# Optimization experiments

Measured on AMD Instinct MI355X. Metric: run time of the kernel, lower is better.

## Reference

```python
import jax, jax.numpy as jnp
import numpy as np

SIGMA = (2.0, 5.0, 10.0, 20.0, 40.0, 60.0)  # RBF bandwidths from __init__
MAX_SEG = 16  # static upper bound on number of class segments (== n classes in gt)


def setup_inputs() -> dict:
    key = jax.random.key(0)
    k1, k2, k3 = jax.random.split(key, 3)
    B, C, H, W = 1, 128, 64, 64
    predict = jax.random.normal(k1, (B, C, H, W), dtype=jnp.float32)
    target = jax.random.normal(k2, (B, C, H, W), dtype=jnp.float32)
    # sorted_randint -> contiguous variable-size class segments, as the torch loop assumes
    gt = jnp.sort(jax.random.randint(k3, (B * H * W,), 0, MAX_SEG)).reshape(B, H, W)
    ignore_mask = jnp.ones((B, H, W), dtype=bool)  # all pixels visible
    return {"predict": predict, "target": target, "gt": gt, "ignore_mask": ignore_mask}


def _sqdist(a, b):
    # ||a_i - b_j||^2 ; prob_mat in the original is -0.5 * this
    aa = jnp.sum(a * a, axis=1)
    bb = jnp.sum(b * b, axis=1)
    return aa[:, None] + bb[None, :] - 2.0 * (a @ b.T)


def reference(predict, target, gt, ignore_mask):
    d = predict.shape[1]
    # [B,C,H,W] -> [V,C]; ignore_mask is all True so visible set == all pixels
    pf = predict.transpose(0, 2, 3, 1).reshape(-1, d)
    tf = target.transpose(0, 2, 3, 1).reshape(-1, d)
    cls = gt.reshape(-1)

    # segment id = index of contiguous class run (what the Python boundary loop computes)
    boundary = (cls[1:] != cls[:-1]).astype(jnp.int32)
    seg = jnp.concatenate([jnp.zeros((1,), jnp.int32), jnp.cumsum(boundary)])
    counts = jax.ops.segment_sum(jnp.ones(seg.shape, predict.dtype), seg, num_segments=MAX_SEG)

    # pairwise squared distances within/between predict and target (shared across segments)
    Dpp = _sqdist(pf, pf)
    Dtt = _sqdist(tf, tf)
    Dpt = _sqdist(pf, tf)

    # Per segment with M=N=n: ww is +1/(2n^2) on pp/tt blocks, -1/(2n^2) on cross blocks,
    # and sum over the tp block equals sum over the pt block. So
    # loss_s = (1/(2 n^2)) * sum_bw sum_{i,j in s} (Kpp + Ktt - 2 Kpt)_{ij}
    C = jnp.zeros_like(Dpp)
    for bw in SIGMA:
        inv = -0.5 / bw  # K = exp(prob/bw) = exp(-||x_i-x_j||^2 / (2 bw))
        C = C + jnp.exp(inv * Dpp) + jnp.exp(inv * Dtt) - 2.0 * jnp.exp(inv * Dpt)

    same = seg[:, None] == seg[None, :]
    C = jnp.where(same, C, 0.0)
    seg_tot = jax.ops.segment_sum(jnp.sum(C, axis=1), seg, num_segments=MAX_SEG)

    denom = jnp.maximum(2.0 * counts * counts, 1.0)
    loss_s = jnp.where(counts > 0, seg_tot / denom, 0.0)
    pos = loss_s > 0
    loss_s = jnp.where(pos, jnp.sqrt(jnp.where(pos, loss_s, 1.0)), 0.0)  # sqrt(loss) if >0 else 0

    class_count = jnp.sum(counts > 0).astype(predict.dtype)
    return jnp.sum(loss_s) / class_count
```

## Files before the change

### kernel.cpp

```cpp
#include <hip/hip_runtime.h>
#include <math.h>

#define NCLS 16
#define TS   64
#define CH   32
#define PAD  36
#define NB   512
#define PIXB 16

typedef float vfloat4 __attribute__((ext_vector_type(4), aligned(4)));

struct Ctl {
    int   counts[NCLS];
    int   starts[NCLS + 1];
    int   tpc[NCLS];
    int   pairBase[NCLS + 1];
    float classSum[NCLS];
};

__global__ __launch_bounds__(256) void prep_kernel(
    const float* __restrict__ P, const float* __restrict__ T,
    const int* __restrict__ gt, int V, int D,
    Ctl* __restrict__ ctl,
    float* __restrict__ normP, float* __restrict__ normT,
    int nbNorm) {
    const int b = blockIdx.x;
    const int t = threadIdx.x;
    if (b < nbNorm) {
        __shared__ float pP[16][PIXB + 1], pT[16][PIXB + 1];
        const int pix = t & (PIXB - 1);
        const int dl  = t >> 4;
        const int v   = b * PIXB + pix;
        float np = 0.f, nt = 0.f;
        if (v < V) {
            #pragma unroll 4
            for (int d = dl; d < D; d += 16) {
                float x = P[(long)d * V + v]; np += x * x;
                float y = T[(long)d * V + v]; nt += y * y;
            }
        }
        pP[dl][pix] = np; pT[dl][pix] = nt;
        __syncthreads();
        if (t < PIXB && b * PIXB + t < V) {
            float sp = 0.f, st = 0.f;
            #pragma unroll
            for (int k = 0; k < 16; ++k) { sp += pP[k][t]; st += pT[k][t]; }
            normP[b * PIXB + t] = sp;
            normT[b * PIXB + t] = st;
        }
    } else {
        if (t < NCLS) {
            int lo = 0, hi = V;
            while (lo < hi) {
                int mid = (lo + hi) >> 1;
                if (gt[mid] < t) lo = mid + 1; else hi = mid;
            }
            ctl->starts[t] = lo;
            ctl->classSum[t] = 0.0f;
        }
        if (t == 0) ctl->starts[NCLS] = V;
        __syncthreads();
        if (t == 0) {
            int pb = 0;
            for (int c = 0; c < NCLS; ++c) {
                int n = ctl->starts[c + 1] - ctl->starts[c];
                ctl->counts[c] = n;
                int tp = (n + TS - 1) / TS;
                ctl->tpc[c] = tp;
                ctl->pairBase[c] = pb;
                pb += tp * (tp + 1) / 2;
            }
            ctl->pairBase[NCLS] = pb;
        }
    }
}

__global__ __launch_bounds__(256) void mmd_kernel(
    const float* __restrict__ P, const float* __restrict__ T,
    int V, int D, const Ctl* __restrict__ ctl,
    const float* __restrict__ normP, const float* __restrict__ normT,
    float* __restrict__ classSum)
{
    __shared__ float sPr[TS][PAD], sTr[TS][PAD];
    __shared__ float sPc[TS][PAD], sTc[TS][PAD];
    __shared__ float wsum[4];

    const int t  = threadIdx.x;
    const int tx = t & 15;
    const int ty = t >> 4;
    const int sd = t >> 3;
    const int qb = t & 7;
    const int W  = ctl->pairBase[NCLS];

    const float invs[6] = {-0.25f, -0.1f, -0.05f, -0.025f, -0.0125f, -1.0f/120.0f};

    for (int w = blockIdx.x; w < W; w += gridDim.x) {
        int c = 0;
        while (ctl->pairBase[c + 1] <= w) ++c;
        const int tp = ctl->tpc[c];
        int rem = w - ctl->pairBase[c];
        int ti = 0;
        while (rem >= tp - ti) { rem -= (tp - ti); ++ti; }
        const int tj     = ti + rem;
        const bool diag  = (ti == tj);
        const int n      = ctl->counts[c];
        const int start  = ctl->starts[c];
        const int i0     = ti * TS;
        const int j0     = tj * TS;

        const int r0 = i0 + 4 * qb;
        const int r1 = i0 + 4 * qb + 32;
        const int c0 = j0 + 4 * qb;
        const int c1 = j0 + 4 * qb + 32;

        vfloat4 vPr0, vPr1, vTr0, vTr1, vPc0, vPc1, vTc0, vTc1;

        auto load_quad = [&](long off, int rb, vfloat4& vP, vfloat4& vT) {
            if (rb + 3 < n) {
                vP = *(const vfloat4*)&P[off + start + rb];
                vT = *(const vfloat4*)&T[off + start + rb];
            } else {
                int a0 = start + min(rb,     n - 1);
                int a1 = start + min(rb + 1, n - 1);
                int a2 = start + min(rb + 2, n - 1);
                int a3 = start + min(rb + 3, n - 1);
                vP = (vfloat4){P[off + a0], P[off + a1], P[off + a2], P[off + a3]};
                vT = (vfloat4){T[off + a0], T[off + a1], T[off + a2], T[off + a3]};
            }
        };
        auto issue_loads = [&](int dcc) {
            const long off = (long)(dcc + sd) * (long)V;
            load_quad(off, r0, vPr0, vTr0);
            load_quad(off, r1, vPr1, vTr1);
            if (!diag) {
                load_quad(off, c0, vPc0, vTc0);
                load_quad(off, c1, vPc1, vTc1);
            }
        };

        const float (*sCp)[PAD] = diag ? sPr : sPc;
        const float (*sCt)[PAD] = diag ? sTr : sTc;

        float dpp[4][4], dtt[4][4], dpt[4][4], dtp[4][4];
        #pragma unroll
        for (int a = 0; a < 4; ++a)
            #pragma unroll
            for (int b = 0; b < 4; ++b)
                { dpp[a][b] = 0.f; dtt[a][b] = 0.f; dpt[a][b] = 0.f; dtp[a][b] = 0.f; }

        issue_loads(0);

        #pragma unroll 1
        for (int dc = 0; dc < D; dc += CH) {
            __syncthreads();
            #pragma unroll
            for (int k = 0; k < 4; ++k) {
                sPr[4*qb +      k][sd] = vPr0[k];
                sPr[4*qb + 32 + k][sd] = vPr1[k];
                sTr[4*qb +      k][sd] = vTr0[k];
                sTr[4*qb + 32 + k][sd] = vTr1[k];
            }
            if (!diag) {
                #pragma unroll
                for (int k = 0; k < 4; ++k) {
                    sPc[4*qb +      k][sd] = vPc0[k];
                    sPc[4*qb + 32 + k][sd] = vPc1[k];
                    sTc[4*qb +      k][sd] = vTc0[k];
                    sTc[4*qb + 32 + k][sd] = vTc1[k];
                }
            }
            __syncthreads();
            if (dc + CH < D)
                issue_loads(dc + CH);

            #pragma unroll 1
            for (int dg = 0; dg < CH; dg += 4) {
                float4 rP[4], rT[4], cP[4], cT[4];
                #pragma unroll
                for (int a = 0; a < 4; ++a) {
                    rP[a] = *(const float4*)&sPr[ty + 16*a][dg];
                    rT[a] = *(const float4*)&sTr[ty + 16*a][dg];
                    cP[a] = *(const float4*)&sCp[tx + 16*a][dg];
                    cT[a] = *(const float4*)&sCt[tx + 16*a][dg];
                }
                #pragma unroll
                for (int a = 0; a < 4; ++a)
                    #pragma unroll
                    for (int b = 0; b < 4; ++b)
                        dpp[a][b] += rP[a].x*cP[b].x + rP[a].y*cP[b].y
                                   + rP[a].z*cP[b].z + rP[a].w*cP[b].w;
                #pragma unroll
                for (int a = 0; a < 4; ++a)
                    #pragma unroll
                    for (int b = 0; b < 4; ++b)
                        dpt[a][b] += rP[a].x*cT[b].x + rP[a].y*cT[b].y
                                   + rP[a].z*cT[b].z + rP[a].w*cT[b].w;
                #pragma unroll
                for (int a = 0; a < 4; ++a)
                    #pragma unroll
                    for (int b = 0; b < 4; ++b)
                        dtt[a][b] += rT[a].x*cT[b].x + rT[a].y*cT[b].y
                                   + rT[a].z*cT[b].z + rT[a].w*cT[b].w;
                #pragma unroll
                for (int a = 0; a < 4; ++a)
                    #pragma unroll
                    for (int b = 0; b < 4; ++b)
                        dtp[a][b] += rT[a].x*cP[b].x + rT[a].y*cP[b].y
                                   + rT[a].z*cP[b].z + rT[a].w*cP[b].w;
            }
        }

        const float f = diag ? 1.0f : 2.0f;
        float total = 0.0f;
        #pragma unroll
        for (int a = 0; a < 4; ++a) {
            const int ii = i0 + ty + 16*a;
            if (ii < n) {
                const float nPi = normP[start + ii];
                const float nTi = normT[start + ii];
                #pragma unroll
                for (int b = 0; b < 4; ++b) {
                    const int jj = j0 + tx + 16*b;
                    if (jj < n) {
                        const float nPj = normP[start + jj];
                        const float nTj = normT[start + jj];
                        float Dpp = nPi + nPj - 2.0f * dpp[a][b];
                        float Dtt = nTi + nTj - 2.0f * dtt[a][b];
                        float Dpt = nPi + nTj - 2.0f * dpt[a][b];
                        float Dtp = nTi + nPj - 2.0f * dtp[a][b];
                        float s6 = 0.0f;
                        #pragma unroll
                        for (int s = 0; s < 6; ++s) {
                            s6 += __expf(invs[s] * Dpp) + __expf(invs[s] * Dtt)
                                - __expf(invs[s] * Dpt) - __expf(invs[s] * Dtp);
                        }
                        total += f * s6;
                    }
                }
            }
        }

        #pragma unroll
        for (int off = 32; off > 0; off >>= 1)
            total += __shfl_down(total, off, 64);
        if ((t & 63) == 0) wsum[t >> 6] = total;
        __syncthreads();
        if (t == 0)
            atomicAdd(&classSum[c], wsum[0] + wsum[1] + wsum[2] + wsum[3]);
    }
}

__global__ void finalize_kernel(const int* __restrict__ counts,
                                const float* __restrict__ classSum,
                                float* __restrict__ out) {
    if (threadIdx.x == 0) {
        float loss = 0.0f;
        int k = 0;
        for (int c = 0; c < NCLS; ++c) {
            int n = counts[c];
            if (n > 0) {
                ++k;
                float fn    = (float)n;
                float denom = fmaxf(2.0f * fn * fn, 1.0f);
                float l     = classSum[c] / denom;
                if (l > 0.0f) loss += sqrtf(l);
            }
        }
        out[0] = (k > 0) ? (loss / (float)k) : 0.0f;
    }
}

extern "C" void kernel_launch(void* const* d_in, const int* in_sizes, int n_in,
                              void* d_out, int out_size, void* d_ws, size_t ws_size,
                              hipStream_t stream) {
    const float* predict = (const float*)d_in[0];
    const float* target  = (const float*)d_in[1];
    const int*   gt      = (const int*)d_in[2];

    const int V = in_sizes[2];
    const int D = in_sizes[0] / V;

    Ctl* ctl = (Ctl*)d_ws;
    size_t normOff = (sizeof(Ctl) + 15) & ~(size_t)15;
    float* normP = (float*)((char*)d_ws + normOff);
    float* normT = normP + V;
    float* classSum = (float*)((char*)d_ws + offsetof(Ctl, classSum));

    int nbNorm = (V + PIXB - 1) / PIXB;
    prep_kernel<<<nbNorm + 1, 256, 0, stream>>>(predict, target, gt, V, D,
                                                ctl, normP, normT, nbNorm);

    mmd_kernel<<<NB, 256, 0, stream>>>(predict, target, V, D, ctl,
                                       normP, normT, classSum);

    finalize_kernel<<<1, 64, 0, stream>>>(ctl->counts, classSum, (float*)d_out);
}
```

Before: 100.5 us.

## Shrink MMD tiles to 32x32 with single-wavefront blocks and drop register prefetch

Halves the pair-tile size to 32 and runs each tile with one 64-thread wavefront, doubling the grid to 1024 blocks. This gives finer-grained work items, better load balance across the small variable-size class segments, and less wasted work on partial tiles near the diagonal. The block reduction becomes a single wavefront shuffle plus atomic, with no shared-memory partial sums. In exchange, the register prefetch of the next channel chunk is removed, so global loads are no longer overlapped with compute, and each block reuses less data per load.

```diff
diff --git a/kernel.cpp b/kernel.cpp
--- a/kernel.cpp
+++ b/kernel.cpp
@@ -2,10 +2,10 @@
 #include <math.h>
 
 #define NCLS 16
-#define TS   64
+#define TS   32
 #define CH   32
 #define PAD  36
-#define NB   512
+#define NB   1024
 #define PIXB 16
 
 typedef float vfloat4 __attribute__((ext_vector_type(4), aligned(4)));
@@ -75,7 +75,7 @@
     }
 }
 
-__global__ __launch_bounds__(256) void mmd_kernel(
+__global__ __launch_bounds__(64) void mmd_kernel(
     const float* __restrict__ P, const float* __restrict__ T,
     int V, int D, const Ctl* __restrict__ ctl,
     const float* __restrict__ normP, const float* __restrict__ normT,
@@ -83,13 +83,12 @@
 {
     __shared__ float sPr[TS][PAD], sTr[TS][PAD];
     __shared__ float sPc[TS][PAD], sTc[TS][PAD];
-    __shared__ float wsum[4];
 
     const int t  = threadIdx.x;
-    const int tx = t & 15;
-    const int ty = t >> 4;
+    const int tx = t & 7;
+    const int ty = t >> 3;
+    const int sq = t & 7;
     const int sd = t >> 3;
-    const int qb = t & 7;
     const int W  = ctl->pairBase[NCLS];
 
     const float invs[6] = {-0.25f, -0.1f, -0.05f, -0.025f, -0.0125f, -1.0f/120.0f};
@@ -108,12 +107,8 @@
         const int i0     = ti * TS;
         const int j0     = tj * TS;
 
-        const int r0 = i0 + 4 * qb;
-        const int r1 = i0 + 4 * qb + 32;
-        const int c0 = j0 + 4 * qb;
-        const int c1 = j0 + 4 * qb + 32;
-
-        vfloat4 vPr0, vPr1, vTr0, vTr1, vPc0, vPc1, vTc0, vTc1;
+        const int rq = i0 + 4 * sq;
+        const int cq = j0 + 4 * sq;
 
         auto load_quad = [&](long off, int rb, vfloat4& vP, vfloat4& vT) {
             if (rb + 3 < n) {
@@ -128,15 +123,6 @@
                 vT = (vfloat4){T[off + a0], T[off + a1], T[off + a2], T[off + a3]};
             }
         };
-        auto issue_loads = [&](int dcc) {
-            const long off = (long)(dcc + sd) * (long)V;
-            load_quad(off, r0, vPr0, vTr0);
-            load_quad(off, r1, vPr1, vTr1);
-            if (!diag) {
-                load_quad(off, c0, vPc0, vTc0);
-                load_quad(off, c1, vPc1, vTc1);
-            }
-        };
 
         const float (*sCp)[PAD] = diag ? sPr : sPc;
         const float (*sCt)[PAD] = diag ? sTr : sTc;
@@ -148,40 +134,41 @@
             for (int b = 0; b < 4; ++b)
                 { dpp[a][b] = 0.f; dtt[a][b] = 0.f; dpt[a][b] = 0.f; dtp[a][b] = 0.f; }
 
-        issue_loads(0);
-
         #pragma unroll 1
         for (int dc = 0; dc < D; dc += CH) {
             __syncthreads();
-            #pragma unroll
-            for (int k = 0; k < 4; ++k) {
-                sPr[4*qb +      k][sd] = vPr0[k];
-                sPr[4*qb + 32 + k][sd] = vPr1[k];
-                sTr[4*qb +      k][sd] = vTr0[k];
-                sTr[4*qb + 32 + k][sd] = vTr1[k];
-            }
-            if (!diag) {
+            #pragma unroll 1
+            for (int m = 0; m < 4; ++m) {
+                const int  dd  = sd + 8 * m;
+                const long off = (long)(dc + dd) * (long)V;
+                vfloat4 pR, tR;
+                load_quad(off, rq, pR, tR);
                 #pragma unroll
                 for (int k = 0; k < 4; ++k) {
-                    sPc[4*qb +      k][sd] = vPc0[k];
-                    sPc[4*qb + 32 + k][sd] = vPc1[k];
-                    sTc[4*qb +      k][sd] = vTc0[k];
-                    sTc[4*qb + 32 + k][sd] = vTc1[k];
+                    sPr[4*sq + k][dd] = pR[k];
+                    sTr[4*sq + k][dd] = tR[k];
+                }
+                if (!diag) {
+                    vfloat4 pC, tC;
+                    load_quad(off, cq, pC, tC);
+                    #pragma unroll
+                    for (int k = 0; k < 4; ++k) {
+                        sPc[4*sq + k][dd] = pC[k];
+                        sTc[4*sq + k][dd] = tC[k];
+                    }
                 }
             }
             __syncthreads();
-            if (dc + CH < D)
-                issue_loads(dc + CH);
 
             #pragma unroll 1
             for (int dg = 0; dg < CH; dg += 4) {
                 float4 rP[4], rT[4], cP[4], cT[4];
                 #pragma unroll
                 for (int a = 0; a < 4; ++a) {
-                    rP[a] = *(const float4*)&sPr[ty + 16*a][dg];
-                    rT[a] = *(const float4*)&sTr[ty + 16*a][dg];
-                    cP[a] = *(const float4*)&sCp[tx + 16*a][dg];
-                    cT[a] = *(const float4*)&sCt[tx + 16*a][dg];
+                    rP[a] = *(const float4*)&sPr[ty + 8*a][dg];
+                    rT[a] = *(const float4*)&sTr[ty + 8*a][dg];
+                    cP[a] = *(const float4*)&sCp[tx + 8*a][dg];
+                    cT[a] = *(const float4*)&sCt[tx + 8*a][dg];
                 }
                 #pragma unroll
                 for (int a = 0; a < 4; ++a)
@@ -214,13 +201,13 @@
         float total = 0.0f;
         #pragma unroll
         for (int a = 0; a < 4; ++a) {
-            const int ii = i0 + ty + 16*a;
+            const int ii = i0 + ty + 8*a;
             if (ii < n) {
                 const float nPi = normP[start + ii];
                 const float nTi = normT[start + ii];
                 #pragma unroll
                 for (int b = 0; b < 4; ++b) {
-                    const int jj = j0 + tx + 16*b;
+                    const int jj = j0 + tx + 8*b;
                     if (jj < n) {
                         const float nPj = normP[start + jj];
                         const float nTj = normT[start + jj];
@@ -243,10 +230,9 @@
         #pragma unroll
         for (int off = 32; off > 0; off >>= 1)
             total += __shfl_down(total, off, 64);
-        if ((t & 63) == 0) wsum[t >> 6] = total;
+        if (t == 0)
+            atomicAdd(&classSum[c], total);
         __syncthreads();
-        if (t == 0)
-            atomicAdd(&classSum[c], wsum[0] + wsum[1] + wsum[2] + wsum[3]);
     }
 }
 
@@ -290,8 +276,8 @@
     prep_kernel<<<nbNorm + 1, 256, 0, stream>>>(predict, target, gt, V, D,
                                                 ctl, normP, normT, nbNorm);
 
-    mmd_kernel<<<NB, 256, 0, stream>>>(predict, target, V, D, ctl,
-                                       normP, normT, classSum);
+    mmd_kernel<<<NB, 64, 0, stream>>>(predict, target, V, D, ctl,
+                                      normP, normT, classSum);
 
     finalize_kernel<<<1, 64, 0, stream>>>(ctl->counts, classSum, (float*)d_out);
 }
```

Result: slower. 105.5 us (+4.9%).
